# Kernel tuning notes

Measured on AMD Instinct MI355X. Metric: run time of the kernel, lower is better.

## Reference

```python
import jax, jax.numpy as jnp
import numpy as np

N = 2000
E = 128
H = 8
DH = E // H
K = 32  # max_neighbors
CLAMP = 1e4


def _sanitize(t):
    t = jnp.nan_to_num(t, nan=0.0, posinf=CLAMP, neginf=-CLAMP)
    return jnp.clip(t, -CLAMP, CLAMP)


def _layernorm(h, g, b, eps=1e-5):
    mu = h.mean(-1, keepdims=True)
    var = ((h - mu) ** 2).mean(-1, keepdims=True)
    return (h - mu) * jax.lax.rsqrt(var + eps) * g + b


def setup_inputs() -> dict:
    key = jax.random.key(0)
    ks = jax.random.split(key, 8)
    x = jax.random.normal(ks[0], (N, E), dtype=jnp.float32)
    coords9 = jax.random.normal(ks[1], (N, 9), dtype=jnp.float32)
    prompt_signal = jax.random.normal(ks[2], (E,), dtype=jnp.float32)
    pe_w = jax.random.normal(ks[3], (3, 32), dtype=jnp.float32) / np.sqrt(3.0)
    pe_b = jnp.zeros((32,), jnp.float32)
    pe_g = jnp.ones((32,), jnp.float32)
    pe_bt = jnp.zeros((32,), jnp.float32)
    in_w = jax.random.normal(ks[4], (3 * E, E), dtype=jnp.float32) / np.sqrt(E)
    in_b = jnp.zeros((3 * E,), jnp.float32)
    out_w = jax.random.normal(ks[5], (E, E), dtype=jnp.float32) / np.sqrt(E)
    out_b = jnp.zeros((E,), jnp.float32)
    return {"x": x, "coords9": coords9, "prompt_signal": prompt_signal,
            "pe_w": pe_w, "pe_b": pe_b, "pe_g": pe_g, "pe_bt": pe_bt,
            "in_w": in_w, "in_b": in_b, "out_w": out_w, "out_b": out_b}


def reference(x, coords9, prompt_signal, pe_w, pe_b, pe_g, pe_bt, in_w, in_b, out_w, out_b):
    n = x.shape[0]
    verts = coords9.reshape(n, 3, 3)
    cent = verts.mean(axis=1)  # (N,3)

    # pairwise centroid distances (only geo-relation channel that affects the output;
    # cos_angles/area_ratios/boundary_sharing feed geo_bias which is dead code in forward)
    diff = cent[:, None, :] - cent[None, :, :]
    dist = jnp.sqrt(jnp.sum(diff * diff, axis=-1) + 1e-20)  # (N,N)

    # positional encoder: Linear(3,32) -> GELU(exact) -> LayerNorm(32)
    pe = jax.nn.gelu(cent @ pe_w + pe_b, approximate=False)
    pe = _layernorm(pe, pe_g, pe_bt)  # (N,32)

    prompt_enhanced = x + prompt_signal[None, :]
    pos_enhanced = jnp.concatenate([prompt_enhanced[:, : 3 * E // 4], pe], axis=-1)  # (N,128)

    # top-K nearest neighbors -> additive attention mask (0 for kept, -inf-like otherwise)
    _, topk_idx = jax.lax.top_k(-dist, K)  # (N,K) smallest distances
    big_neg = jnp.float32(-1e9)
    attn_mask = jnp.full((n, n), big_neg, dtype=jnp.float32)
    attn_mask = attn_mask.at[jnp.arange(n)[:, None], topk_idx].set(0.0)

    # nn.MultiheadAttention (self-attention, eval mode -> no dropout)
    qkv = pos_enhanced @ in_w.T + in_b  # (N,3E)
    q, k, v = jnp.split(qkv, 3, axis=-1)
    q = q.reshape(n, H, DH).transpose(1, 0, 2)  # (H,N,DH)
    k = k.reshape(n, H, DH).transpose(1, 0, 2)
    v = v.reshape(n, H, DH).transpose(1, 0, 2)
    scores = jnp.einsum('hnd,hmd->hnm', q, k) / np.sqrt(DH) + attn_mask[None]
    probs = jax.nn.softmax(scores, axis=-1)
    o = jnp.einsum('hnm,hmd->hnd', probs, v)  # (H,N,DH)
    o = o.transpose(1, 0, 2).reshape(n, E)
    out = o @ out_w.T + out_b
    return _sanitize(out)
```

## Files before the change

### kernel.cpp

```cpp
#include <hip/hip_runtime.h>
#include <math.h>

#define N_NODES 2000
#define E_DIM   128
#define QKV_W   384
#define LDA     36

__global__ __launch_bounds__(256) void prep_qkv_kernel(
    const float* __restrict__ x, const float* __restrict__ coords9,
    const float* __restrict__ ps, const float* __restrict__ pe_w,
    const float* __restrict__ pe_b, const float* __restrict__ pe_g,
    const float* __restrict__ pe_bt, const float* __restrict__ in_w,
    const float* __restrict__ in_b,
    float* __restrict__ cx_, float* __restrict__ cy_, float* __restrict__ cz_,
    float* __restrict__ qkv)
{
    __shared__ __align__(16) float As[E_DIM * LDA];
    int tid = threadIdx.x;
    int rt = blockIdx.x / 3, ct = blockIdx.x % 3;
    int rbase = rt * 32, cbase = ct * 128;
    int g = tid >> 5, lane = tid & 31;

    #pragma unroll
    for (int rr = 0; rr < 4; ++rr) {
        int rl = rr * 8 + g;
        int row = rbase + rl;
        bool vr = (row < N_NODES);
        float cx = 0.f, cy = 0.f, cz = 0.f;
        if (vr) {
            const float* c9 = coords9 + row * 9;
            cx = (c9[0] + c9[3] + c9[6]) * (1.0f / 3.0f);
            cy = (c9[1] + c9[4] + c9[7]) * (1.0f / 3.0f);
            cz = (c9[2] + c9[5] + c9[8]) * (1.0f / 3.0f);
        }
        if (ct == 0 && vr && lane == 0) { cx_[row] = cx; cy_[row] = cy; cz_[row] = cz; }

        #pragma unroll
        for (int k = 0; k < 3; ++k) {
            int c = lane + 32 * k;
            float v = vr ? (x[row * E_DIM + c] + ps[c]) : 0.f;
            As[c * LDA + rl] = v;
        }

        int j = lane;
        float h = cx * pe_w[j] + cy * pe_w[32 + j] + cz * pe_w[64 + j] + pe_b[j];
        float ge = 0.5f * h * (1.0f + erff(h * 0.7071067811865476f));
        float s = ge;
        #pragma unroll
        for (int m = 16; m >= 1; m >>= 1) s += __shfl_xor(s, m);
        float mu = s * (1.0f / 32.0f);
        float d = ge - mu;
        float v2 = d * d;
        #pragma unroll
        for (int m = 16; m >= 1; m >>= 1) v2 += __shfl_xor(v2, m);
        float var = v2 * (1.0f / 32.0f);
        float y = d * (1.0f / sqrtf(var + 1e-5f)) * pe_g[j] + pe_bt[j];
        As[(96 + j) * LDA + rl] = vr ? y : 0.f;
    }
    __syncthreads();

    int cg = tid & 31, rg = tid >> 5;
    int c0 = cbase + cg * 4, r0 = rg * 4;
    float acc[4][4];
    #pragma unroll
    for (int i = 0; i < 4; ++i)
        #pragma unroll
        for (int jj = 0; jj < 4; ++jj) acc[i][jj] = 0.f;

    for (int k0 = 0; k0 < 128; k0 += 4) {
        float4 a0 = *(const float4*)&As[(k0 + 0) * LDA + r0];
        float4 a1 = *(const float4*)&As[(k0 + 1) * LDA + r0];
        float4 a2 = *(const float4*)&As[(k0 + 2) * LDA + r0];
        float4 a3 = *(const float4*)&As[(k0 + 3) * LDA + r0];
        #pragma unroll
        for (int ci = 0; ci < 4; ++ci) {
            float4 b = *(const float4*)&in_w[(c0 + ci) * E_DIM + k0];
            acc[0][ci] += a0.x * b.x + a1.x * b.y + a2.x * b.z + a3.x * b.w;
            acc[1][ci] += a0.y * b.x + a1.y * b.y + a2.y * b.z + a3.y * b.w;
            acc[2][ci] += a0.z * b.x + a1.z * b.y + a2.z * b.z + a3.z * b.w;
            acc[3][ci] += a0.w * b.x + a1.w * b.y + a2.w * b.z + a3.w * b.w;
        }
    }

    #pragma unroll
    for (int ri = 0; ri < 4; ++ri) {
        int row = rbase + r0 + ri;
        if (row < N_NODES) {
            float4 o4;
            o4.x = acc[ri][0] + in_b[c0 + 0];
            o4.y = acc[ri][1] + in_b[c0 + 1];
            o4.z = acc[ri][2] + in_b[c0 + 2];
            o4.w = acc[ri][3] + in_b[c0 + 3];
            *(float4*)&qkv[row * QKV_W + c0] = o4;
        }
    }
}

__device__ __forceinline__ float sanitize(float v)
{
    v = (v == v) ? v : 0.f;
    return fminf(fmaxf(v, -1e4f), 1e4f);
}

__global__ __launch_bounds__(256) void attn_proj_kernel(
    const float* __restrict__ cx_, const float* __restrict__ cy_,
    const float* __restrict__ cz_, const float* __restrict__ qkv,
    const float* __restrict__ out_w, const float* __restrict__ out_b,
    float* __restrict__ out)
{
    __shared__ __align__(16) unsigned int hist[4][256];
    __shared__ int eqIdx[4][256];
    __shared__ unsigned int eqKey[4][256];
    __shared__ int topk[4][32];
    __shared__ int cnt[4][2];
    __shared__ __align__(16) float qs[4][128];
    __shared__ __align__(16) float pr[4][256];
    __shared__ __align__(16) float os[4][128];

    int tid = threadIdx.x;
    int lane = tid & 63, w = tid >> 6;
    int row = blockIdx.x * 4 + w;

    float cix = cx_[row], ciy = cy_[row], ciz = cz_[row];

    unsigned int kb[32];
    float lmin = __int_as_float(0x7f800000);
    float lmax = __int_as_float(0xff800000);
    {
        #pragma clang fp contract(off)
        #pragma unroll
        for (int it = 0; it < 32; ++it) {
            int j = lane + 64 * it;
            float key = __int_as_float(0x7f800000);
            if (j < N_NODES) {
                float dx = cix - cx_[j];
                float dy = ciy - cy_[j];
                float dz = ciz - cz_[j];
                float a = dx * dx;
                float b2 = dy * dy;
                float c = dz * dz;
                float d2 = ((a + b2) + c) + 1e-20f;
                key = sqrtf(d2);
                lmin = fminf(lmin, key);
                lmax = fmaxf(lmax, key);
            }
            kb[it] = __float_as_uint(key);
        }
    }
    #pragma unroll
    for (int m = 32; m >= 1; m >>= 1) {
        lmin = fminf(lmin, __shfl_xor(lmin, m));
        lmax = fmaxf(lmax, __shfl_xor(lmax, m));
    }
    float lo = lmin;
    float scale = 255.0f / fmaxf(lmax - lmin, 1e-30f);

    *(uint4*)&hist[w][4 * lane] = make_uint4(0u, 0u, 0u, 0u);
    if (lane == 0) { cnt[w][0] = 0; cnt[w][1] = 0; }
    __builtin_amdgcn_wave_barrier();
    #pragma unroll
    for (int it = 0; it < 32; ++it) {
        int j = lane + 64 * it;
        if (j < N_NODES) {
            float key = __uint_as_float(kb[it]);
            int bin = (int)((key - lo) * scale);
            bin = min(max(bin, 0), 255);
            atomicAdd(&hist[w][bin], 1u);
        }
    }
    __builtin_amdgcn_wave_barrier();

    uint4 h4 = *(const uint4*)&hist[w][4 * lane];
    int s0 = (int)h4.x;
    int s1 = s0 + (int)h4.y;
    int s2 = s1 + (int)h4.z;
    int tot = s2 + (int)h4.w;
    int incl = tot;
    #pragma unroll
    for (int dd = 1; dd < 64; dd <<= 1) {
        int u = __shfl_up(incl, dd);
        if (lane >= dd) incl += u;
    }
    int excl = incl - tot;
    int c0 = excl + s0, c1 = excl + s1, c2 = excl + s2, c3 = excl + tot;
    int cand = 256, candN = 0;
    if (excl < 32 && c0 >= 32)      { cand = 4 * lane;     candN = excl; }
    else if (c0 < 32 && c1 >= 32)   { cand = 4 * lane + 1; candN = c0; }
    else if (c1 < 32 && c2 >= 32)   { cand = 4 * lane + 2; candN = c1; }
    else if (c2 < 32 && c3 >= 32)   { cand = 4 * lane + 3; candN = c2; }
    int candV = (cand << 8) | candN;
    #pragma unroll
    for (int m = 32; m >= 1; m >>= 1) candV = min(candV, __shfl_xor(candV, m));
    int b = candV >> 8;
    int req = 32 - (candV & 255);

    #pragma unroll
    for (int it = 0; it < 32; ++it) {
        int j = lane + 64 * it;
        if (j < N_NODES) {
            float key = __uint_as_float(kb[it]);
            int bin = (int)((key - lo) * scale);
            bin = min(max(bin, 0), 255);
            if (bin < b) {
                int p = atomicAdd(&cnt[w][0], 1);
                topk[w][p] = j;
            } else if (bin == b) {
                int e = atomicAdd(&cnt[w][1], 1);
                if (e < 256) { eqIdx[w][e] = j; eqKey[w][e] = kb[it]; }
            }
        }
    }
    qs[w][lane]      = qkv[row * QKV_W + lane];
    qs[w][lane + 64] = qkv[row * QKV_W + lane + 64];
    __builtin_amdgcn_wave_barrier();

    int eq = min(cnt[w][1], 256);
    for (int e = lane; e < eq; e += 64) {
        int myIdx = eqIdx[w][e];
        unsigned int myKey = eqKey[w][e];
        int rank = 0;
        for (int u = 0; u < eq; ++u) {
            unsigned int ku = eqKey[w][u];
            rank += (ku < myKey || (ku == myKey && eqIdx[w][u] < myIdx)) ? 1 : 0;
        }
        if (rank < req) {
            int p = atomicAdd(&cnt[w][0], 1);
            topk[w][p] = myIdx;
        }
    }
    __builtin_amdgcn_wave_barrier();

    int tk[32];
    #pragma unroll
    for (int sl = 0; sl < 32; ++sl) tk[sl] = topk[w][sl];

    #pragma unroll
    for (int pp = 0; pp < 4; ++pp) {
        int p = lane + 64 * pp;
        int hh = p >> 5, sl = p & 31;
        int jj = tk[sl];
        const float4* kp = (const float4*)&qkv[jj * QKV_W + 128 + hh * 16];
        const float4* qp = (const float4*)&qs[w][hh * 16];
        float s = 0.f;
        #pragma unroll
        for (int i = 0; i < 4; ++i) {
            float4 kv = kp[i], qv = qp[i];
            s += qv.x * kv.x + qv.y * kv.y + qv.z * kv.z + qv.w * kv.w;
        }
        s *= 0.25f;
        float m = s;
        #pragma unroll
        for (int msk = 16; msk >= 1; msk >>= 1) m = fmaxf(m, __shfl_xor(m, msk));
        float pe = expf(s - m);
        float su = pe;
        #pragma unroll
        for (int msk = 16; msk >= 1; msk >>= 1) su += __shfl_xor(su, msk);
        pr[w][p] = pe / su;
    }
    __builtin_amdgcn_wave_barrier();

    #pragma unroll
    for (int cc = 0; cc < 2; ++cc) {
        int c = lane + 64 * cc;
        int hh = c >> 4;
        float acc = 0.f;
        #pragma unroll
        for (int sl = 0; sl < 32; ++sl) {
            acc += pr[w][hh * 32 + sl] * qkv[tk[sl] * QKV_W + 256 + c];
        }
        os[w][c] = acc;
    }
    __builtin_amdgcn_wave_barrier();

    #pragma unroll
    for (int cc = 0; cc < 2; ++cc) {
        int c = lane + 64 * cc;
        const float* wr = out_w + c * E_DIM;
        float a = 0.f;
        #pragma unroll
        for (int e = 0; e < 128; e += 4) {
            float4 w4 = *(const float4*)&wr[e];
            float4 o4 = *(const float4*)&os[w][e];
            a += o4.x * w4.x + o4.y * w4.y + o4.z * w4.z + o4.w * w4.w;
        }
        out[row * E_DIM + c] = sanitize(a + out_b[c]);
    }
}

extern "C" void kernel_launch(void* const* d_in, const int* in_sizes, int n_in,
                              void* d_out, int out_size, void* d_ws, size_t ws_size,
                              hipStream_t stream)
{
    const float* x      = (const float*)d_in[0];
    const float* coords = (const float*)d_in[1];
    const float* ps     = (const float*)d_in[2];
    const float* pe_w   = (const float*)d_in[3];
    const float* pe_b   = (const float*)d_in[4];
    const float* pe_g   = (const float*)d_in[5];
    const float* pe_bt  = (const float*)d_in[6];
    const float* in_w   = (const float*)d_in[7];
    const float* in_b   = (const float*)d_in[8];
    const float* out_w  = (const float*)d_in[9];
    const float* out_b  = (const float*)d_in[10];
    float* out = (float*)d_out;

    float* ws  = (float*)d_ws;
    float* cxp = ws;
    float* cyp = ws + 2048;
    float* czp = ws + 4096;
    float* qkvb = ws + 6144;

    prep_qkv_kernel<<<189, 256, 0, stream>>>(x, coords, ps, pe_w, pe_b, pe_g, pe_bt,
                                             in_w, in_b, cxp, cyp, czp, qkvb);
    attn_proj_kernel<<<500, 256, 0, stream>>>(cxp, cyp, czp, qkvb, out_w, out_b, out);
}
```

Baseline: 137.9 us.

## Split each row's neighbor search across four waves and merge candidates block-wide

The attention kernel previously gave each wave one full row, scanning all 2000 distances serially. Now each block handles one row: the four waves each take a quarter of the columns and pick a local top-32 by histogram. A block-wide rank sort then merges the 128 candidates into the final 32 neighbors, and the grid grows from 500 to 2000 blocks. This cuts per-wave serial work and raises occupancy on the GPU, at the cost of extra __syncthreads, a 128-way rank merge, and later phases that use only half the threads.

```diff
diff --git a/kernel.cpp b/kernel.cpp
--- a/kernel.cpp
+++ b/kernel.cpp
@@ -109,30 +109,34 @@
     float* __restrict__ out)
 {
     __shared__ __align__(16) unsigned int hist[4][256];
-    __shared__ int eqIdx[4][256];
-    __shared__ unsigned int eqKey[4][256];
-    __shared__ int topk[4][32];
+    __shared__ int eqIdx[4][128];
+    __shared__ unsigned int eqKey[4][128];
     __shared__ int cnt[4][2];
-    __shared__ __align__(16) float qs[4][128];
-    __shared__ __align__(16) float pr[4][256];
-    __shared__ __align__(16) float os[4][128];
+    __shared__ unsigned int candKey[128];
+    __shared__ int candIdx[128];
+    __shared__ int topk[32];
+    __shared__ __align__(16) float qs[128];
+    __shared__ float pr[256];
+    __shared__ __align__(16) float os[128];
 
     int tid = threadIdx.x;
+    int row = blockIdx.x;
     int lane = tid & 63, w = tid >> 6;
-    int row = blockIdx.x * 4 + w;
 
     float cix = cx_[row], ciy = cy_[row], ciz = cz_[row];
 
-    unsigned int kb[32];
+    unsigned int kb[8];
+    bool valid[8];
     float lmin = __int_as_float(0x7f800000);
     float lmax = __int_as_float(0xff800000);
     {
         #pragma clang fp contract(off)
         #pragma unroll
-        for (int it = 0; it < 32; ++it) {
-            int j = lane + 64 * it;
+        for (int it = 0; it < 8; ++it) {
+            int j = 64 * w + lane + 256 * it;
+            valid[it] = (j < N_NODES);
             float key = __int_as_float(0x7f800000);
-            if (j < N_NODES) {
+            if (valid[it]) {
                 float dx = cix - cx_[j];
                 float dy = ciy - cy_[j];
                 float dz = ciz - cz_[j];
@@ -158,15 +162,17 @@
     *(uint4*)&hist[w][4 * lane] = make_uint4(0u, 0u, 0u, 0u);
     if (lane == 0) { cnt[w][0] = 0; cnt[w][1] = 0; }
     __builtin_amdgcn_wave_barrier();
-    #pragma unroll
-    for (int it = 0; it < 32; ++it) {
-        int j = lane + 64 * it;
-        if (j < N_NODES) {
+    int bins[8];
+    #pragma unroll
+    for (int it = 0; it < 8; ++it) {
+        int bin = 255;
+        if (valid[it]) {
             float key = __uint_as_float(kb[it]);
-            int bin = (int)((key - lo) * scale);
+            bin = (int)((key - lo) * scale);
             bin = min(max(bin, 0), 255);
             atomicAdd(&hist[w][bin], 1u);
         }
+        bins[it] = bin;
     }
     __builtin_amdgcn_wave_barrier();
 
@@ -184,10 +190,10 @@
     int excl = incl - tot;
     int c0 = excl + s0, c1 = excl + s1, c2 = excl + s2, c3 = excl + tot;
     int cand = 256, candN = 0;
-    if (excl < 32 && c0 >= 32)      { cand = 4 * lane;     candN = excl; }
-    else if (c0 < 32 && c1 >= 32)   { cand = 4 * lane + 1; candN = c0; }
-    else if (c1 < 32 && c2 >= 32)   { cand = 4 * lane + 2; candN = c1; }
-    else if (c2 < 32 && c3 >= 32)   { cand = 4 * lane + 3; candN = c2; }
+    if (excl < 32 && c0 >= 32)    { cand = 4 * lane;     candN = excl; }
+    else if (c0 < 32 && c1 >= 32) { cand = 4 * lane + 1; candN = c0; }
+    else if (c1 < 32 && c2 >= 32) { cand = 4 * lane + 2; candN = c1; }
+    else if (c2 < 32 && c3 >= 32) { cand = 4 * lane + 3; candN = c2; }
     int candV = (cand << 8) | candN;
     #pragma unroll
     for (int m = 32; m >= 1; m >>= 1) candV = min(candV, __shfl_xor(candV, m));
@@ -195,26 +201,23 @@
     int req = 32 - (candV & 255);
 
     #pragma unroll
-    for (int it = 0; it < 32; ++it) {
-        int j = lane + 64 * it;
-        if (j < N_NODES) {
-            float key = __uint_as_float(kb[it]);
-            int bin = (int)((key - lo) * scale);
-            bin = min(max(bin, 0), 255);
+    for (int it = 0; it < 8; ++it) {
+        if (valid[it]) {
+            int bin = bins[it];
+            int j = 64 * w + lane + 256 * it;
             if (bin < b) {
                 int p = atomicAdd(&cnt[w][0], 1);
-                topk[w][p] = j;
+                candIdx[w * 32 + p] = j;
+                candKey[w * 32 + p] = kb[it];
             } else if (bin == b) {
                 int e = atomicAdd(&cnt[w][1], 1);
-                if (e < 256) { eqIdx[w][e] = j; eqKey[w][e] = kb[it]; }
+                if (e < 128) { eqIdx[w][e] = j; eqKey[w][e] = kb[it]; }
             }
         }
     }
-    qs[w][lane]      = qkv[row * QKV_W + lane];
-    qs[w][lane + 64] = qkv[row * QKV_W + lane + 64];
     __builtin_amdgcn_wave_barrier();
 
-    int eq = min(cnt[w][1], 256);
+    int eq = min(cnt[w][1], 128);
     for (int e = lane; e < eq; e += 64) {
         int myIdx = eqIdx[w][e];
         unsigned int myKey = eqKey[w][e];
@@ -225,22 +228,32 @@
         }
         if (rank < req) {
             int p = atomicAdd(&cnt[w][0], 1);
-            topk[w][p] = myIdx;
-        }
-    }
-    __builtin_amdgcn_wave_barrier();
-
-    int tk[32];
-    #pragma unroll
-    for (int sl = 0; sl < 32; ++sl) tk[sl] = topk[w][sl];
-
-    #pragma unroll
-    for (int pp = 0; pp < 4; ++pp) {
-        int p = lane + 64 * pp;
-        int hh = p >> 5, sl = p & 31;
-        int jj = tk[sl];
+            candIdx[w * 32 + p] = myIdx;
+            candKey[w * 32 + p] = myKey;
+        }
+    }
+    __syncthreads();
+
+    if (tid < 128) {
+        unsigned int myKey = candKey[tid];
+        int myIdx = candIdx[tid];
+        int rank = 0;
+        #pragma unroll 4
+        for (int u = 0; u < 128; ++u) {
+            unsigned int ku = candKey[u];
+            rank += (ku < myKey || (ku == myKey && candIdx[u] < myIdx)) ? 1 : 0;
+        }
+        if (rank < 32) topk[rank] = myIdx;
+    } else {
+        qs[tid - 128] = qkv[row * QKV_W + (tid - 128)];
+    }
+    __syncthreads();
+
+    {
+        int hh = tid >> 5, j = tid & 31;
+        int jj = topk[j];
         const float4* kp = (const float4*)&qkv[jj * QKV_W + 128 + hh * 16];
-        const float4* qp = (const float4*)&qs[w][hh * 16];
+        const float4* qp = (const float4*)&qs[hh * 16];
         float s = 0.f;
         #pragma unroll
         for (int i = 0; i < 4; ++i) {
@@ -255,35 +268,32 @@
         float su = pe;
         #pragma unroll
         for (int msk = 16; msk >= 1; msk >>= 1) su += __shfl_xor(su, msk);
-        pr[w][p] = pe / su;
-    }
-    __builtin_amdgcn_wave_barrier();
-
-    #pragma unroll
-    for (int cc = 0; cc < 2; ++cc) {
-        int c = lane + 64 * cc;
-        int hh = c >> 4;
+        pr[tid] = pe / su;
+    }
+    __syncthreads();
+
+    if (tid < 128) {
+        int hh = tid >> 4;
         float acc = 0.f;
         #pragma unroll
-        for (int sl = 0; sl < 32; ++sl) {
-            acc += pr[w][hh * 32 + sl] * qkv[tk[sl] * QKV_W + 256 + c];
-        }
-        os[w][c] = acc;
-    }
-    __builtin_amdgcn_wave_barrier();
-
-    #pragma unroll
-    for (int cc = 0; cc < 2; ++cc) {
-        int c = lane + 64 * cc;
-        const float* wr = out_w + c * E_DIM;
+        for (int j = 0; j < 32; ++j) {
+            int jj = topk[j];
+            acc += pr[hh * 32 + j] * qkv[jj * QKV_W + 256 + tid];
+        }
+        os[tid] = acc;
+    }
+    __syncthreads();
+
+    if (tid < 128) {
+        const float* wr = out_w + tid * E_DIM;
         float a = 0.f;
         #pragma unroll
         for (int e = 0; e < 128; e += 4) {
             float4 w4 = *(const float4*)&wr[e];
-            float4 o4 = *(const float4*)&os[w][e];
+            float4 o4 = *(const float4*)&os[e];
             a += o4.x * w4.x + o4.y * w4.y + o4.z * w4.z + o4.w * w4.w;
         }
-        out[row * E_DIM + c] = sanitize(a + out_b[c]);
+        out[row * E_DIM + tid] = sanitize(a + out_b[tid]);
     }
 }
 
@@ -312,5 +322,5 @@
 
     prep_qkv_kernel<<<189, 256, 0, stream>>>(x, coords, ps, pe_w, pe_b, pe_g, pe_bt,
                                              in_w, in_b, cxp, cyp, czp, qkvb);
-    attn_proj_kernel<<<500, 256, 0, stream>>>(cxp, cyp, czp, qkvb, out_w, out_b, out);
+    attn_proj_kernel<<<2000, 256, 0, stream>>>(cxp, cyp, czp, qkvb, out_w, out_b, out);
 }
```

Result: faster. 127.3 us (-7.7%).
